# Optimization experiments

Measured on AMD Instinct MI355X. Metric: run time of the kernel, lower is better.

The kernel has to match this reference:

```python
import jax, jax.numpy as jnp
import numpy as np

EPS = 1e-8  # torch.nn.CosineSimilarity default eps

def setup_inputs() -> dict:
    key = jax.random.key(0)
    k1, k2 = jax.random.split(key)
    B, R, T, D = 256, 36, 64, 1024
    img_feats = jax.random.normal(k1, (B, R, D), dtype=jnp.float32)
    cap_feats = jax.random.normal(k2, (B, T, D), dtype=jnp.float32)
    cap_mask = jnp.ones((B, T), dtype=jnp.float32)  # unused by the original forward
    return {"img_feats": img_feats, "cap_feats": cap_feats, "cap_mask": cap_mask}

def reference(img_feats, cap_feats, cap_mask):
    # img_feats: (B, R, D); cap_feats: (B, T, D)
    # cosine similarity between every region r and every caption word t:
    # scores[b, r, t] = (img[b,r] . cap[b,t]) / max(||img[b,r]|| * ||cap[b,t]||, eps)
    dots = jnp.einsum('brd,btd->brt', img_feats, cap_feats)
    img_norm = jnp.linalg.norm(img_feats, axis=-1)  # (B, R)
    cap_norm = jnp.linalg.norm(cap_feats, axis=-1)  # (B, T)
    denom = jnp.maximum(img_norm[:, :, None] * cap_norm[:, None, :], EPS)
    scores = dots / denom  # (B, R, T)
    # softmax over regions (dim=1 in the original)
    attn = jax.nn.softmax(scores, axis=1)  # (B, R, T)
    # weighted sum over regions -> per-word image representation (B, T, D)
    img_cap_reps = jnp.einsum('brt,brd->btd', attn, img_feats)
    return img_cap_reps
```

## Files before the change

### kernel.cpp

```cpp
#include <hip/hip_runtime.h>

#define RREG 36
#define TTOK 64
#define DDIM 1024

#define BUFSZ  28672
#define IMGOFF 16384
#define SMEMSZ 86016

typedef __attribute__((ext_vector_type(4))) float f32x4;
typedef __attribute__((ext_vector_type(8))) short bf16x8;

__device__ __forceinline__ unsigned short f2bf(float x) {
  unsigned int u = __float_as_uint(x);
  u += 0x7fffu + ((u >> 16) & 1u);
  return (unsigned short)(u >> 16);
}

__device__ __forceinline__ bf16x8 cvt8(float4 a, float4 b) {
  bf16x8 r;
  r[0] = (short)f2bf(a.x); r[1] = (short)f2bf(a.y);
  r[2] = (short)f2bf(a.z); r[3] = (short)f2bf(a.w);
  r[4] = (short)f2bf(b.x); r[5] = (short)f2bf(b.y);
  r[6] = (short)f2bf(b.z); r[7] = (short)f2bf(b.w);
  return r;
}

__device__ __forceinline__ float sq8(float4 a, float4 b) {
  return a.x*a.x + a.y*a.y + a.z*a.z + a.w*a.w +
         b.x*b.x + b.y*b.y + b.z*b.z + b.w*b.w;
}

__device__ __forceinline__ void async16(void* lds, const void* g) {
  __builtin_amdgcn_global_load_lds(
      (const __attribute__((address_space(1))) unsigned int*)g,
      (__attribute__((address_space(3))) unsigned int*)lds, 16, 0, 0);
}

__device__ __forceinline__ void issue_hc(
    unsigned char* smem, int hc, int wave, int lane,
    const unsigned char* capb8, const unsigned char* imgb8,
    int srow, int ssw, int irc) {
  unsigned char* buf = smem + (hc % 3) * BUFSZ;
  async16(buf + (wave << 10) + (lane << 4),
          capb8 + ((size_t)srow << 12) + ((size_t)hc << 8) + ssw);
  if (wave < 12)
    async16(buf + IMGOFF + (wave << 10) + (lane << 4),
            imgb8 + ((size_t)irc << 12) + ((size_t)hc << 8) + ssw);
}

__global__ __launch_bounds__(1024, 4) void scan_fused(
    const float* __restrict__ img, const float* __restrict__ cap,
    float* __restrict__ out) {
  __shared__ __align__(16) unsigned char smem[SMEMSZ];

  float* ssc  = (float*)(smem);
  float* satt = (float*)(smem + 13056);
  float* sni  = (float*)(smem + 23296);
  float* snc  = (float*)(smem + 23488);

  const int tid  = threadIdx.x;
  const int lane = tid & 63;
  const int wave = tid >> 6;
  const int fm   = lane & 15;
  const int kq   = lane >> 4;
  const int b    = blockIdx.x;

  const float* imgb = img + (size_t)b * RREG * DDIM;
  const float* capb = cap + (size_t)b * TTOK * DDIM;
  float*       outb = out + (size_t)b * TTOK * DDIM;
  const unsigned char* capb8 = (const unsigned char*)capb;
  const unsigned char* imgb8 = (const unsigned char*)imgb;

  const int srow = (wave << 2) + (lane >> 4);
  const int soff = (lane & 15) << 4;
  const int ssw  = soff ^ ((srow & 7) << 4);
  const int irc  = srow < RREG ? srow : srow - RREG;

  const int mt = wave >> 2;
  const int nt = wave & 3;

  f32x4 acc = {0.f, 0.f, 0.f, 0.f};
  float nI = 0.f, nC = 0.f;

  issue_hc(smem, 0, wave, lane, capb8, imgb8, srow, ssw, irc);
  issue_hc(smem, 1, wave, lane, capb8, imgb8, srow, ssw, irc);

#pragma unroll
  for (int c = 0; c < 16; ++c) {
    if (c < 15) {
      if (wave < 12) asm volatile("s_waitcnt vmcnt(2)" ::: "memory");
      else           asm volatile("s_waitcnt vmcnt(1)" ::: "memory");
    } else {
      asm volatile("s_waitcnt vmcnt(0)" ::: "memory");
    }
    __builtin_amdgcn_s_barrier();
    asm volatile("" ::: "memory");
    if (c < 14)
      issue_hc(smem, c + 2, wave, lane, capb8, imgb8, srow, ssw, irc);
    if (wave < 12) {
      const unsigned char* buf = smem + (c % 3) * BUFSZ;
      const int arow = mt * 16 + fm;
      const int brow = nt * 16 + fm;
      const unsigned char* ap = buf + IMGOFF + (arow << 8);
      const unsigned char* bp = buf + (brow << 8);
      const int sA = (arow & 7) << 4;
      const int sB = (brow & 7) << 4;
#pragma unroll
      for (int ks = 0; ks < 2; ++ks) {
        const int cb = (kq << 5) + (ks << 7);
        float4 a0 = *(const float4*)(ap + ((cb     ) ^ sA));
        float4 a1 = *(const float4*)(ap + ((cb + 16) ^ sA));
        float4 b0 = *(const float4*)(bp + ((cb     ) ^ sB));
        float4 b1 = *(const float4*)(bp + ((cb + 16) ^ sB));
        if (nt == 0) nI += sq8(a0, a1);
        if (mt == 0) nC += sq8(b0, b1);
        acc = __builtin_amdgcn_mfma_f32_16x16x32_bf16(
            cvt8(a0, a1), cvt8(b0, b1), acc, 0, 0, 0);
      }
    }
  }

  __builtin_amdgcn_s_barrier();
  asm volatile("" ::: "memory");

  if (wave < 12) {
#pragma unroll
    for (int i = 0; i < 4; ++i)
      ssc[(mt * 16 + kq * 4 + i) * 66 + nt * 16 + fm] = acc[i];
    nI += __shfl_xor(nI, 16); nI += __shfl_xor(nI, 32);
    nC += __shfl_xor(nC, 16); nC += __shfl_xor(nC, 32);
    const int ar = mt * 16 + fm, br = nt * 16 + fm;
    if (nt == 0 && kq == 0 && ar < RREG) sni[ar] = sqrtf(nI);
    if (mt == 0 && kq == 0)              snc[br] = sqrtf(nC);
  }

  float ic[RREG];
#pragma unroll
  for (int r = 0; r < RREG; ++r) ic[r] = imgb[r * DDIM + tid];

  asm volatile("s_waitcnt lgkmcnt(0)" ::: "memory");
  __builtin_amdgcn_s_barrier();
  asm volatile("" ::: "memory");

  {
    const int tok = (wave << 2) | (lane >> 4);
    const int rr  = lane & 15;
    const float cnv = snc[tok];
    const float s0v = ssc[rr * 66 + tok]        / fmaxf(sni[rr] * cnv, 1e-8f);
    const float s1v = ssc[(rr + 16) * 66 + tok] / fmaxf(sni[rr + 16] * cnv, 1e-8f);
    float s2v = -1e30f;
    if (rr < 4) s2v = ssc[(rr + 32) * 66 + tok] / fmaxf(sni[rr + 32] * cnv, 1e-8f);
    float mx = fmaxf(fmaxf(s0v, s1v), s2v);
#pragma unroll
    for (int o = 8; o > 0; o >>= 1) mx = fmaxf(mx, __shfl_xor(mx, o));
    const float e0 = __expf(s0v - mx);
    const float e1 = __expf(s1v - mx);
    const float e2 = (rr < 4) ? __expf(s2v - mx) : 0.f;
    float sm = e0 + e1 + e2;
#pragma unroll
    for (int o = 8; o > 0; o >>= 1) sm += __shfl_xor(sm, o);
    const float rinv = 1.f / sm;
    satt[tok * 40 + rr]      = e0 * rinv;
    satt[tok * 40 + rr + 16] = e1 * rinv;
    if (rr < 4) satt[tok * 40 + rr + 32] = e2 * rinv;
  }

  asm volatile("s_waitcnt lgkmcnt(0)" ::: "memory");
  __builtin_amdgcn_s_barrier();
  asm volatile("" ::: "memory");

#pragma unroll 2
  for (int t = 0; t < TTOK; ++t) {
    const float4* ap4 = (const float4*)(satt + t * 40);
    float p0 = 0.f, p1 = 0.f, p2 = 0.f, p3 = 0.f;
#pragma unroll
    for (int r4 = 0; r4 < 9; ++r4) {
      float4 a4 = ap4[r4];
      p0 += a4.x * ic[r4 * 4 + 0];
      p1 += a4.y * ic[r4 * 4 + 1];
      p2 += a4.z * ic[r4 * 4 + 2];
      p3 += a4.w * ic[r4 * 4 + 3];
    }
    outb[(size_t)t * DDIM + tid] = (p0 + p1) + (p2 + p3);
  }
}

extern "C" void kernel_launch(void* const* d_in, const int* in_sizes, int n_in,
                              void* d_out, int out_size, void* d_ws, size_t ws_size,
                              hipStream_t stream) {
  const float* img = (const float*)d_in[0];
  const float* cap = (const float*)d_in[1];
  float* out = (float*)d_out;
  scan_fused<<<dim3(256), dim3(1024), 0, stream>>>(img, cap, out);
}
```

Measured before the change: 178.9 us.

## Stage bf16 image and caption tiles in LDS via register loads, reuse image for output

Replaces the async global-to-LDS fp32 triple-buffered pipeline with register loads that convert to bf16 and store into padded LDS buffers. Norms are now computed during staging. The whole image block is kept resident in LDS as bf16 and reused for the final weighted sum instead of re-reading it from global memory. This cuts LDS footprint and removes the second global image read, but loses the async overlap. The output now uses bf16-rounded image values, which reduces accuracy.

New measurement: 173.6 us. -2.9%, faster.

```diff
diff --git a/kernel.cpp b/kernel.cpp
--- a/kernel.cpp
+++ b/kernel.cpp
@@ -4,9 +4,17 @@
 #define TTOK 64
 #define DDIM 1024
 
-#define BUFSZ  28672
-#define IMGOFF 16384
-#define SMEMSZ 86016
+#define IMG_STRIDE 1032
+#define CAP_STRIDE 264
+#define IMG_BYTES    (RREG * IMG_STRIDE * 2)
+#define CAPBUF_BYTES (TTOK * CAP_STRIDE * 2)
+#define OFF_CAP0  IMG_BYTES
+#define OFF_CAP1  (OFF_CAP0 + CAPBUF_BYTES)
+#define OFF_SSC   (OFF_CAP1 + CAPBUF_BYTES)
+#define OFF_SNI   (OFF_SSC + 48 * 66 * 4)
+#define OFF_SNC   (OFF_SNI + 192)
+#define SMEMSZ    (OFF_SNC + 256)
+#define OFF_SATT  OFF_CAP0
 
 typedef __attribute__((ext_vector_type(4))) float f32x4;
 typedef __attribute__((ext_vector_type(8))) short bf16x8;
@@ -26,27 +34,13 @@
   return r;
 }
 
-__device__ __forceinline__ float sq8(float4 a, float4 b) {
-  return a.x*a.x + a.y*a.y + a.z*a.z + a.w*a.w +
-         b.x*b.x + b.y*b.y + b.z*b.z + b.w*b.w;
+__device__ __forceinline__ float sq4(float4 a) {
+  return a.x*a.x + a.y*a.y + a.z*a.z + a.w*a.w;
 }
 
-__device__ __forceinline__ void async16(void* lds, const void* g) {
-  __builtin_amdgcn_global_load_lds(
-      (const __attribute__((address_space(1))) unsigned int*)g,
-      (__attribute__((address_space(3))) unsigned int*)lds, 16, 0, 0);
-}
-
-__device__ __forceinline__ void issue_hc(
-    unsigned char* smem, int hc, int wave, int lane,
-    const unsigned char* capb8, const unsigned char* imgb8,
-    int srow, int ssw, int irc) {
-  unsigned char* buf = smem + (hc % 3) * BUFSZ;
-  async16(buf + (wave << 10) + (lane << 4),
-          capb8 + ((size_t)srow << 12) + ((size_t)hc << 8) + ssw);
-  if (wave < 12)
-    async16(buf + IMGOFF + (wave << 10) + (lane << 4),
-            imgb8 + ((size_t)irc << 12) + ((size_t)hc << 8) + ssw);
+__device__ __forceinline__ void lds_barrier() {
+  asm volatile("s_waitcnt lgkmcnt(0)" ::: "memory");
+  __builtin_amdgcn_s_barrier();
 }
 
 __global__ __launch_bounds__(1024, 4) void scan_fused(
@@ -54,10 +48,11 @@
     float* __restrict__ out) {
   __shared__ __align__(16) unsigned char smem[SMEMSZ];
 
-  float* ssc  = (float*)(smem);
-  float* satt = (float*)(smem + 13056);
-  float* sni  = (float*)(smem + 23296);
-  float* snc  = (float*)(smem + 23488);
+  unsigned short* simg = (unsigned short*)smem;
+  float* ssc  = (float*)(smem + OFF_SSC);
+  float* sni  = (float*)(smem + OFF_SNI);
+  float* snc  = (float*)(smem + OFF_SNC);
+  float* satt = (float*)(smem + OFF_SATT);
 
   const int tid  = threadIdx.x;
   const int lane = tid & 63;
@@ -69,79 +64,78 @@
   const float* imgb = img + (size_t)b * RREG * DDIM;
   const float* capb = cap + (size_t)b * TTOK * DDIM;
   float*       outb = out + (size_t)b * TTOK * DDIM;
-  const unsigned char* capb8 = (const unsigned char*)capb;
-  const unsigned char* imgb8 = (const unsigned char*)imgb;
 
-  const int srow = (wave << 2) + (lane >> 4);
-  const int soff = (lane & 15) << 4;
-  const int ssw  = soff ^ ((srow & 7) << 4);
-  const int irc  = srow < RREG ? srow : srow - RREG;
+  const int ctr = tid >> 4;
+  const int cc  = (tid & 15) << 4;
+  const bool hasI = (tid < 16 * RREG);
 
   const int mt = wave >> 2;
   const int nt = wave & 3;
+  const int arow = mt * 16 + fm;
+  const int brow = nt * 16 + fm;
+  const bool avld = (arow < RREG);
 
   f32x4 acc = {0.f, 0.f, 0.f, 0.f};
-  float nI = 0.f, nC = 0.f;
-
-  issue_hc(smem, 0, wave, lane, capb8, imgb8, srow, ssw, irc);
-  issue_hc(smem, 1, wave, lane, capb8, imgb8, srow, ssw, irc);
+  float nC = 0.f, nI = 0.f;
+  const bf16x8 zb = {0, 0, 0, 0, 0, 0, 0, 0};
 
 #pragma unroll
-  for (int c = 0; c < 16; ++c) {
-    if (c < 15) {
-      if (wave < 12) asm volatile("s_waitcnt vmcnt(2)" ::: "memory");
-      else           asm volatile("s_waitcnt vmcnt(1)" ::: "memory");
-    } else {
-      asm volatile("s_waitcnt vmcnt(0)" ::: "memory");
+  for (int p = 0; p < 4; ++p) {
+    {
+      const float* cp = capb + (size_t)ctr * DDIM + p * 256 + cc;
+      float4 c0 = *(const float4*)(cp + 0);
+      float4 c1 = *(const float4*)(cp + 4);
+      float4 c2 = *(const float4*)(cp + 8);
+      float4 c3 = *(const float4*)(cp + 12);
+      float4 i0, i1, i2, i3;
+      if (hasI) {
+        const float* ip = imgb + (size_t)ctr * DDIM + p * 256 + cc;
+        i0 = *(const float4*)(ip + 0);
+        i1 = *(const float4*)(ip + 4);
+        i2 = *(const float4*)(ip + 8);
+        i3 = *(const float4*)(ip + 12);
+      }
+      nC += sq4(c0) + sq4(c1) + sq4(c2) + sq4(c3);
+      unsigned short* cw = (unsigned short*)(smem + OFF_CAP0 + (p & 1) * CAPBUF_BYTES)
+                           + ctr * CAP_STRIDE + cc;
+      *(bf16x8*)(cw + 0) = cvt8(c0, c1);
+      *(bf16x8*)(cw + 8) = cvt8(c2, c3);
+      if (hasI) {
+        nI += sq4(i0) + sq4(i1) + sq4(i2) + sq4(i3);
+        unsigned short* iw = simg + ctr * IMG_STRIDE + p * 256 + cc;
+        *(bf16x8*)(iw + 0) = cvt8(i0, i1);
+        *(bf16x8*)(iw + 8) = cvt8(i2, i3);
+      }
     }
-    __builtin_amdgcn_s_barrier();
-    asm volatile("" ::: "memory");
-    if (c < 14)
-      issue_hc(smem, c + 2, wave, lane, capb8, imgb8, srow, ssw, irc);
+    lds_barrier();
     if (wave < 12) {
-      const unsigned char* buf = smem + (c % 3) * BUFSZ;
-      const int arow = mt * 16 + fm;
-      const int brow = nt * 16 + fm;
-      const unsigned char* ap = buf + IMGOFF + (arow << 8);
-      const unsigned char* bp = buf + (brow << 8);
-      const int sA = (arow & 7) << 4;
-      const int sB = (brow & 7) << 4;
+      const unsigned short* ab = simg + arow * IMG_STRIDE + p * 256 + kq * 8;
+      const unsigned short* bb = (const unsigned short*)(smem + OFF_CAP0 + (p & 1) * CAPBUF_BYTES)
+                                 + brow * CAP_STRIDE + kq * 8;
 #pragma unroll
-      for (int ks = 0; ks < 2; ++ks) {
-        const int cb = (kq << 5) + (ks << 7);
-        float4 a0 = *(const float4*)(ap + ((cb     ) ^ sA));
-        float4 a1 = *(const float4*)(ap + ((cb + 16) ^ sA));
-        float4 b0 = *(const float4*)(bp + ((cb     ) ^ sB));
-        float4 b1 = *(const float4*)(bp + ((cb + 16) ^ sB));
-        if (nt == 0) nI += sq8(a0, a1);
-        if (mt == 0) nC += sq8(b0, b1);
-        acc = __builtin_amdgcn_mfma_f32_16x16x32_bf16(
-            cvt8(a0, a1), cvt8(b0, b1), acc, 0, 0, 0);
+      for (int ks = 0; ks < 8; ++ks) {
+        bf16x8 av = avld ? *(const bf16x8*)(ab + ks * 32) : zb;
+        bf16x8 bv = *(const bf16x8*)(bb + ks * 32);
+        acc = __builtin_amdgcn_mfma_f32_16x16x32_bf16(av, bv, acc, 0, 0, 0);
       }
     }
   }
-
-  __builtin_amdgcn_s_barrier();
-  asm volatile("" ::: "memory");
 
   if (wave < 12) {
 #pragma unroll
     for (int i = 0; i < 4; ++i)
       ssc[(mt * 16 + kq * 4 + i) * 66 + nt * 16 + fm] = acc[i];
-    nI += __shfl_xor(nI, 16); nI += __shfl_xor(nI, 32);
-    nC += __shfl_xor(nC, 16); nC += __shfl_xor(nC, 32);
-    const int ar = mt * 16 + fm, br = nt * 16 + fm;
-    if (nt == 0 && kq == 0 && ar < RREG) sni[ar] = sqrtf(nI);
-    if (mt == 0 && kq == 0)              snc[br] = sqrtf(nC);
   }
-
-  float ic[RREG];
 #pragma unroll
-  for (int r = 0; r < RREG; ++r) ic[r] = imgb[r * DDIM + tid];
-
-  asm volatile("s_waitcnt lgkmcnt(0)" ::: "memory");
-  __builtin_amdgcn_s_barrier();
-  asm volatile("" ::: "memory");
+  for (int off = 8; off > 0; off >>= 1) {
+    nC += __shfl_down(nC, off, 16);
+    nI += __shfl_down(nI, off, 16);
+  }
+  if ((tid & 15) == 0) {
+    snc[ctr] = sqrtf(nC);
+    if (hasI) sni[ctr] = sqrtf(nI);
+  }
+  lds_barrier();
 
   {
     const int tok = (wave << 2) | (lane >> 4);
@@ -165,11 +159,14 @@
     satt[tok * 40 + rr + 16] = e1 * rinv;
     if (rr < 4) satt[tok * 40 + rr + 32] = e2 * rinv;
   }
+  lds_barrier();
 
-  asm volatile("s_waitcnt lgkmcnt(0)" ::: "memory");
-  __builtin_amdgcn_s_barrier();
-  asm volatile("" ::: "memory");
-
+  float ic[RREG];
+#pragma unroll
+  for (int r = 0; r < RREG; ++r) {
+    unsigned int u = simg[r * IMG_STRIDE + tid];
+    ic[r] = __uint_as_float(u << 16);
+  }
 #pragma unroll 2
   for (int t = 0; t < TTOK; ++t) {
     const float4* ap4 = (const float4*)(satt + t * 40);
```
